# Kernel optimization log

Measured on AMD Instinct MI355X. Metric: run time of the kernel, lower is better.

The kernel has to match this reference:

```python
import jax, jax.numpy as jnp
import numpy as np

N_NODES = 100000
N_REL = 8
F_IN, F_HID, F_OUT = 64, 64, 32
N_EDGES = 1000000


def rgcn_conv(x, W, root, bias, src, dst, edge_type):
    """PyG RGCNConv with default aggr='mean': out[i] = sum_r mean_{j in N_r(i)} W_r x_j + root x_i + bias."""
    R, _, O = W.shape
    N = x.shape[0]
    # Transform every node under every relation: [R, N, O]
    h = jnp.einsum('nf,rfo->rno', x, W)
    # Gather per-edge messages: [E, O]
    msg = h[edge_type, src]
    # Per-(relation, dst) mean aggregation via combined segment ids
    seg = edge_type * N + dst
    sums = jax.ops.segment_sum(msg, seg, num_segments=R * N).reshape(R, N, O)
    cnt = jax.ops.segment_sum(jnp.ones((msg.shape[0],), msg.dtype), seg,
                              num_segments=R * N).reshape(R, N, 1)
    mean = sums / jnp.maximum(cnt, 1.0)  # empty neighborhoods -> 0
    return mean.sum(axis=0) + x @ root + bias


def setup_inputs() -> dict:
    key = jax.random.key(0)
    ks = jax.random.split(key, 9)
    s = lambda fan: 1.0 / np.sqrt(fan)
    x = jax.random.normal(ks[0], (N_NODES, F_IN), jnp.float32)
    edge_index = jax.random.randint(ks[1], (2, N_EDGES), 0, N_NODES, jnp.int64)
    edge_type = jax.random.randint(ks[2], (N_EDGES,), 0, N_REL, jnp.int64)
    W1 = jax.random.normal(ks[3], (N_REL, F_IN, F_HID), jnp.float32) * s(F_IN)
    root1 = jax.random.normal(ks[4], (F_IN, F_HID), jnp.float32) * s(F_IN)
    b1 = jnp.zeros((F_HID,), jnp.float32)
    W2 = jax.random.normal(ks[5], (N_REL, F_HID, F_OUT), jnp.float32) * s(F_HID)
    root2 = jax.random.normal(ks[6], (F_HID, F_OUT), jnp.float32) * s(F_HID)
    b2 = jnp.zeros((F_OUT,), jnp.float32)
    return {"x": x, "W1": W1, "root1": root1, "b1": b1,
            "W2": W2, "root2": root2, "b2": b2,
            "edge_index": edge_index, "edge_type": edge_type}


def reference(x, W1, root1, b1, W2, root2, b2, edge_index, edge_type):
    src, dst = edge_index[0], edge_index[1]
    # encode (dropout is identity in eval mode)
    h = jax.nn.relu(rgcn_conv(x, W1, root1, b1, src, dst, edge_type))
    z = rgcn_conv(h, W2, root2, b2, src, dst, edge_type)
    # decode: gather-dot-product link scores over the same edge list
    return (z[src] * z[dst]).sum(axis=1)
```

## Files before the change

kernel.cpp:

```cpp
#include <hip/hip_runtime.h>

#define F_IN 64
#define F_HID 64
#define F_OUT 32
#define NREL 8
#define SCAP 6144
#define RCAP 10240
#define MAXBUCK 200
#define PA_PE 16

typedef __attribute__((ext_vector_type(8))) short bfrag;
typedef __attribute__((ext_vector_type(4))) float ffrag;

__device__ inline unsigned short f2bf(float f) {
  unsigned u = __float_as_uint(f);
  unsigned r = (u + 0x7fffu + ((u >> 16) & 1u)) >> 16;
  return (unsigned short)r;
}
__device__ inline unsigned bf16pair(float lo, float hi) {
  return (unsigned)f2bf(lo) | ((unsigned)f2bf(hi) << 16);
}
__device__ inline float bflo(unsigned u) { return __uint_as_float(u << 16); }
__device__ inline float bfhi(unsigned u) { return __uint_as_float(u & 0xffff0000u); }

__device__ inline void acc8(float (&acc)[8], float s, uint4 g) {
  acc[0] += s * bflo(g.x); acc[1] += s * bfhi(g.x);
  acc[2] += s * bflo(g.y); acc[3] += s * bfhi(g.y);
  acc[4] += s * bflo(g.z); acc[5] += s * bfhi(g.z);
  acc[6] += s * bflo(g.w); acc[7] += s * bfhi(g.w);
}
__device__ inline float dot8(uint4 a, uint4 b) {
  return bflo(a.x) * bflo(b.x) + bfhi(a.x) * bfhi(b.x) +
         bflo(a.y) * bflo(b.y) + bfhi(a.y) * bfhi(b.y) +
         bflo(a.z) * bflo(b.z) + bfhi(a.z) * bfhi(b.z) +
         bflo(a.w) * bflo(b.w) + bfhi(a.w) * bfhi(b.w);
}

template <int O>
__device__ inline void wprep_one(int t, const float* __restrict__ W,
                                 const float* __restrict__ root,
                                 unsigned short* __restrict__ Wf) {
  constexpr int CT = O / 16;
  int l = t & 63;
  int s = (t >> 6) & 1;
  int rc = t >> 7;
  int c = rc % CT;
  int r = rc / CT;
  const float* wsrc = (r < NREL) ? W + (size_t)r * 64 * O : root;
  unsigned short* dst = Wf + (size_t)t * 8;
  int col = c * 16 + (l & 15);
  int k0 = s * 32 + ((l >> 4) * 8);
#pragma unroll
  for (int j = 0; j < 8; ++j) dst[j] = f2bf(wsrc[(size_t)(k0 + j) * O + col]);
}

__global__ __launch_bounds__(256) void prep_kernel(
    const float* __restrict__ W1, const float* __restrict__ root1,
    const float* __restrict__ W2, const float* __restrict__ root2,
    unsigned short* __restrict__ wf1, unsigned short* __restrict__ wf2,
    int* __restrict__ gcur, int nbuck) {
  int gid = blockIdx.x * 256 + threadIdx.x;
  const int J1 = (NREL + 1) * (F_HID / 16) * 2 * 64;
  const int J2 = (NREL + 1) * (F_OUT / 16) * 2 * 64;
  if (gid < J1) {
    wprep_one<F_HID>(gid, W1, root1, wf1);
  } else if (gid < J1 + J2) {
    wprep_one<F_OUT>(gid - J1, W2, root2, wf2);
  } else if (gid - J1 - J2 < nbuck) {
    int b = gid - J1 - J2;
    gcur[b] = b * SCAP;
  }
}

__global__ __launch_bounds__(256) void binA_kernel(
    const int* __restrict__ src, const int* __restrict__ dst,
    const int* __restrict__ et, int* __restrict__ gcur,
    unsigned* __restrict__ staging, int E) {
  __shared__ int hist[MAXBUCK * 4];
  __shared__ int wbase[MAXBUCK * 4];
  const int tid = threadIdx.x;
  const int wave = tid >> 6;
  for (int i = tid; i < MAXBUCK * 4; i += 256) hist[i] = 0;
  __syncthreads();
  const int base = blockIdx.x * (256 * PA_PE);
  int dv[PA_PE], rk[PA_PE];
#pragma unroll
  for (int j = 0; j < PA_PE; ++j) {
    int e = base + j * 256 + tid;
    if (e < E) {
      int d = dst[e];
      dv[j] = d;
      rk[j] = atomicAdd(&hist[(d >> 9) * 4 + wave], 1);
    } else {
      dv[j] = -1;
    }
  }
  __syncthreads();
  for (int b = tid; b < MAXBUCK; b += 256) {
    int h0 = hist[b * 4 + 0], h1 = hist[b * 4 + 1];
    int h2 = hist[b * 4 + 2], h3 = hist[b * 4 + 3];
    int tot = h0 + h1 + h2 + h3;
    int gb = tot ? atomicAdd(&gcur[b], tot) : 0;
    wbase[b * 4 + 0] = gb;
    wbase[b * 4 + 1] = gb + h0;
    wbase[b * 4 + 2] = gb + h0 + h1;
    wbase[b * 4 + 3] = gb + h0 + h1 + h2;
  }
  __syncthreads();
#pragma unroll
  for (int j = 0; j < PA_PE; ++j) {
    if (dv[j] >= 0) {
      int e = base + j * 256 + tid;
      unsigned pk = (unsigned)src[e] | ((unsigned)et[e] << 17) |
                    ((unsigned)(dv[j] & 511) << 20);
      staging[wbase[(dv[j] >> 9) * 4 + wave] + rk[j]] = pk;
    }
  }
}

__global__ __launch_bounds__(256) void binB_kernel(
    const unsigned* __restrict__ staging, const int* __restrict__ gcur,
    int2* __restrict__ rec, int* __restrict__ startsA, int* __restrict__ endsA,
    int N) {
  __shared__ int cnt8[512 * 8];
  __shared__ int cur[512];
  __shared__ int tsum[256];
  const int b = blockIdx.x;
  const int tid = threadIdx.x;
  const int n0 = b << 9;
  const int nn = min(512, N - n0);
  const int cnt_b = gcur[b] - b * SCAP;
  const unsigned* st = staging + (size_t)b * SCAP;
  for (int i = tid; i < 512 * 8; i += 256) cnt8[i] = 0;
  __syncthreads();
  for (int i = tid; i < cnt_b; i += 256) {
    unsigned e = st[i];
    atomicAdd(&cnt8[((e >> 20) & 511) * 8 + ((e >> 17) & 7)], 1);
  }
  __syncthreads();
  const int na = 2 * tid, nb = 2 * tid + 1;
  int deg0 = 0, deg1 = 0;
#pragma unroll
  for (int r = 0; r < 8; ++r) {
    deg0 += cnt8[na * 8 + r];
    deg1 += cnt8[nb * 8 + r];
  }
  const int pd0 = (deg0 + 7) & ~7, pd1 = (deg1 + 7) & ~7;
  tsum[tid] = pd0 + pd1;
  __syncthreads();
  for (int off = 1; off < 256; off <<= 1) {
    int v = (tid >= off) ? tsum[tid - off] : 0;
    __syncthreads();
    tsum[tid] += v;
    __syncthreads();
  }
  const int excl = tsum[tid] - (pd0 + pd1);
  const int s0 = b * RCAP + excl;
  const int s1 = s0 + pd0;
  if (na < nn) { startsA[n0 + na] = s0; endsA[n0 + na] = s0 + pd0; cur[na] = s0; }
  if (nb < nn) { startsA[n0 + nb] = s1; endsA[n0 + nb] = s1 + pd1; cur[nb] = s1; }
  __syncthreads();
  for (int i = tid; i < 512 * 8; i += 256) {
    int cc = cnt8[i];
    ((float*)cnt8)[i] = cc > 0 ? 1.0f / (float)cc : 0.0f;
  }
  __syncthreads();
  for (int i = tid; i < cnt_b; i += 256) {
    unsigned e = st[i];
    int s = e & 0x1FFFF;
    int r = (e >> 17) & 7;
    int dl = (e >> 20) & 511;
    int pos = atomicAdd(&cur[dl], 1);
    rec[pos] = make_int2(r * N + s, ((const int*)cnt8)[dl * 8 + r]);
  }
  __syncthreads();
  if (na < nn) for (int p = cur[na]; p < s0 + pd0; ++p) rec[p] = make_int2(0, 0);
  if (nb < nn) for (int p = cur[nb]; p < s1 + pd1; ++p) rec[p] = make_int2(0, 0);
}

template <int O, bool F32IN>
__global__ __launch_bounds__(256) void mfma_transform_kernel(
    const void* __restrict__ Xv, const unsigned short* __restrict__ Wf,
    unsigned short* __restrict__ H, int N) {
  constexpr int CT = O / 16;
  constexpr int PAD = (O == 32) ? 40 : 72;
  __shared__ unsigned short tile[64 * PAD];
  const int w = threadIdx.x >> 6;
  const int l = threadIdx.x & 63;
  const int nb = blockIdx.x * 64;
  int arow = nb + w * 16 + (l & 15);
  if (arow >= N) arow = N - 1;
  bfrag a0, a1;
  if (F32IN) {
    const float* xf = (const float*)Xv + (size_t)arow * 64 + ((l >> 4) * 8);
    float4 v0 = *(const float4*)(xf);
    float4 v1 = *(const float4*)(xf + 4);
    float4 v2 = *(const float4*)(xf + 32);
    float4 v3 = *(const float4*)(xf + 36);
    a0[0] = (short)f2bf(v0.x); a0[1] = (short)f2bf(v0.y);
    a0[2] = (short)f2bf(v0.z); a0[3] = (short)f2bf(v0.w);
    a0[4] = (short)f2bf(v1.x); a0[5] = (short)f2bf(v1.y);
    a0[6] = (short)f2bf(v1.z); a0[7] = (short)f2bf(v1.w);
    a1[0] = (short)f2bf(v2.x); a1[1] = (short)f2bf(v2.y);
    a1[2] = (short)f2bf(v2.z); a1[3] = (short)f2bf(v2.w);
    a1[4] = (short)f2bf(v3.x); a1[5] = (short)f2bf(v3.y);
    a1[6] = (short)f2bf(v3.z); a1[7] = (short)f2bf(v3.w);
  } else {
    const unsigned short* xp = (const unsigned short*)Xv + (size_t)arow * 64 + ((l >> 4) * 8);
    a0 = *(const bfrag*)(xp);
    a1 = *(const bfrag*)(xp + 32);
  }
  const int row = threadIdx.x >> 2, seg = threadIdx.x & 3;
  for (int r = 0; r < NREL + 1; ++r) {
    const unsigned short* wb = Wf + ((size_t)r * CT * 2 * 64 + l) * 8;
    ffrag acc[CT];
#pragma unroll
    for (int c = 0; c < CT; ++c) {
      bfrag b0 = *(const bfrag*)(wb + (size_t)(c * 2 + 0) * 512);
      bfrag b1 = *(const bfrag*)(wb + (size_t)(c * 2 + 1) * 512);
      ffrag z = {0.f, 0.f, 0.f, 0.f};
      acc[c] = __builtin_amdgcn_mfma_f32_16x16x32_bf16(a0, b0, z, 0, 0, 0);
      acc[c] = __builtin_amdgcn_mfma_f32_16x16x32_bf16(a1, b1, acc[c], 0, 0, 0);
    }
#pragma unroll
    for (int c = 0; c < CT; ++c)
#pragma unroll
      for (int i = 0; i < 4; ++i)
        tile[(w * 16 + (l >> 4) * 4 + i) * PAD + c * 16 + (l & 15)] = f2bf(acc[c][i]);
    __syncthreads();
    if (nb + row < N) {
      if (O == 64) {
        const uint4* sp = (const uint4*)(tile + row * PAD + seg * 16);
        uint4* gp = (uint4*)(H + ((size_t)r * N + nb + row) * 64 + seg * 16);
        gp[0] = sp[0];
        gp[1] = sp[1];
      } else {
        *(uint4*)(H + ((size_t)r * N + nb + row) * O + seg * 8) =
            *(const uint4*)(tile + row * PAD + seg * 8);
      }
    }
    __syncthreads();
  }
}

template <int O, bool RELU>
__global__ __launch_bounds__(256) void csr_agg_kernel(
    const unsigned* __restrict__ H, const int* __restrict__ startsA,
    const int* __restrict__ endsA, const int2* __restrict__ rec,
    const float* __restrict__ bias, unsigned* __restrict__ Y, int N) {
  constexpr int C = O / 8;
  constexpr int NPB = 256 / C;
  constexpr int HROW = O / 2;
  int t = threadIdx.x;
  int n = blockIdx.x * NPB + t / C;
  int c = t % C;
  if (n >= N) return;
  float acc[8];
  uint4 rr = *(const uint4*)(H + ((size_t)(NREL * N) + n) * HROW + c * 4);
  acc[0] = bias[c * 8 + 0] + bflo(rr.x);
  acc[1] = bias[c * 8 + 1] + bfhi(rr.x);
  acc[2] = bias[c * 8 + 2] + bflo(rr.y);
  acc[3] = bias[c * 8 + 3] + bfhi(rr.y);
  acc[4] = bias[c * 8 + 4] + bflo(rr.z);
  acc[5] = bias[c * 8 + 5] + bfhi(rr.z);
  acc[6] = bias[c * 8 + 6] + bflo(rr.w);
  acc[7] = bias[c * 8 + 7] + bfhi(rr.w);
  int p = startsA[n];
  int end = endsA[n];
  for (; p < end; p += 8) {
    int4 e01 = *(const int4*)(rec + p);
    int4 e23 = *(const int4*)(rec + p + 2);
    int4 e45 = *(const int4*)(rec + p + 4);
    int4 e67 = *(const int4*)(rec + p + 6);
    uint4 g0 = *(const uint4*)(H + (size_t)e01.x * HROW + c * 4);
    uint4 g1 = *(const uint4*)(H + (size_t)e01.z * HROW + c * 4);
    uint4 g2 = *(const uint4*)(H + (size_t)e23.x * HROW + c * 4);
    uint4 g3 = *(const uint4*)(H + (size_t)e23.z * HROW + c * 4);
    uint4 g4 = *(const uint4*)(H + (size_t)e45.x * HROW + c * 4);
    uint4 g5 = *(const uint4*)(H + (size_t)e45.z * HROW + c * 4);
    uint4 g6 = *(const uint4*)(H + (size_t)e67.x * HROW + c * 4);
    uint4 g7 = *(const uint4*)(H + (size_t)e67.z * HROW + c * 4);
    acc8(acc, __int_as_float(e01.y), g0);
    acc8(acc, __int_as_float(e01.w), g1);
    acc8(acc, __int_as_float(e23.y), g2);
    acc8(acc, __int_as_float(e23.w), g3);
    acc8(acc, __int_as_float(e45.y), g4);
    acc8(acc, __int_as_float(e45.w), g5);
    acc8(acc, __int_as_float(e67.y), g6);
    acc8(acc, __int_as_float(e67.w), g7);
  }
  if (RELU) {
#pragma unroll
    for (int j = 0; j < 8; ++j) acc[j] = fmaxf(acc[j], 0.f);
  }
  uint4 o;
  o.x = bf16pair(acc[0], acc[1]);
  o.y = bf16pair(acc[2], acc[3]);
  o.z = bf16pair(acc[4], acc[5]);
  o.w = bf16pair(acc[6], acc[7]);
  *(uint4*)(Y + (size_t)n * HROW + c * 4) = o;
}

__global__ __launch_bounds__(256) void decode_kernel(
    const unsigned* __restrict__ Z, const int* __restrict__ src,
    const int* __restrict__ dst, float* __restrict__ out, int E) {
  int e = blockIdx.x * blockDim.x + threadIdx.x;
  if (e >= E) return;
  const uint4* zs = (const uint4*)(Z + (size_t)src[e] * 16);
  const uint4* zd = (const uint4*)(Z + (size_t)dst[e] * 16);
  uint4 a0 = zs[0], a1 = zs[1], a2 = zs[2], a3 = zs[3];
  uint4 b0 = zd[0], b1 = zd[1], b2 = zd[2], b3 = zd[3];
  out[e] = dot8(a0, b0) + dot8(a1, b1) + dot8(a2, b2) + dot8(a3, b3);
}

extern "C" void kernel_launch(void* const* d_in, const int* in_sizes, int n_in,
                              void* d_out, int out_size, void* d_ws, size_t ws_size,
                              hipStream_t stream) {
  const float* x     = (const float*)d_in[0];
  const float* W1    = (const float*)d_in[1];
  const float* root1 = (const float*)d_in[2];
  const float* b1    = (const float*)d_in[3];
  const float* W2    = (const float*)d_in[4];
  const float* root2 = (const float*)d_in[5];
  const float* b2    = (const float*)d_in[6];
  const int*   ei    = (const int*)d_in[7];
  const int*   et    = (const int*)d_in[8];

  const int N = in_sizes[0] / F_IN;
  const int E = in_sizes[8];
  const int nbuck = (N + 511) >> 9;
  const int* srcp = ei;
  const int* dstp = ei + E;

  char* ws = (char*)d_ws;
  int*            gcur    = (int*)(ws + 0);
  unsigned*       staging = (unsigned*)(ws + 4096);
  int*            startsA = (int*)(ws + 4919296);
  int*            endsA   = (int*)(ws + 5319296);
  int2*           rec     = (int2*)(ws + 5719296);
  unsigned short* wf1     = (unsigned short*)(ws + 21775616);
  unsigned short* wf2     = (unsigned short*)(ws + 21849344);
  unsigned short* h       = (unsigned short*)(ws + 21886208);
  unsigned short* hmid    = (unsigned short*)(ws + 137086208);
  unsigned short* z       = (unsigned short*)(ws + 149886208);

  prep_kernel<<<28, 256, 0, stream>>>(W1, root1, W2, root2, wf1, wf2, gcur, nbuck);
  binA_kernel<<<(E + 256 * PA_PE - 1) / (256 * PA_PE), 256, 0, stream>>>(
      srcp, dstp, et, gcur, staging, E);
  binB_kernel<<<nbuck, 256, 0, stream>>>(staging, gcur, rec, startsA, endsA, N);

  mfma_transform_kernel<F_HID, true>
      <<<(N + 63) / 64, 256, 0, stream>>>(x, wf1, h, N);
  csr_agg_kernel<F_HID, true>
      <<<(N + 31) / 32, 256, 0, stream>>>((const unsigned*)h, startsA, endsA, rec,
                                          b1, (unsigned*)hmid, N);

  mfma_transform_kernel<F_OUT, false>
      <<<(N + 63) / 64, 256, 0, stream>>>(hmid, wf2, h, N);
  csr_agg_kernel<F_OUT, false>
      <<<(N + 63) / 64, 256, 0, stream>>>((const unsigned*)h, startsA, endsA, rec,
                                          b2, (unsigned*)z, N);

  decode_kernel<<<(E + 255) / 256, 256, 0, stream>>>((const unsigned*)z, srcp, dstp,
                                                     (float*)d_out, E);
}
```

Baseline: 174.2 us.

## Store MFMA outputs directly in permuted column layout, dropping LDS staging

The transform kernel now writes MFMA accumulators straight to global memory in an interleaved feature order, which removes the shared-memory tile and both block barriers per relation. Downstream consumers are adapted: layer-2 weights get their K dimension permuted to match layer-1's permuted hidden layout, and the aggregation kernel reads the bias through the same permutation. The trade is narrower global stores (8 or 4 bytes per lane) in exchange for no LDS round trip or synchronization. It relies on the decode dot product being invariant to the permuted output column order.

Measured after the change: 169.5 us. 2.7% less time.

```diff
diff --git a/kernel.cpp b/kernel.cpp
--- a/kernel.cpp
+++ b/kernel.cpp
@@ -36,7 +36,7 @@
          bflo(a.w) * bflo(b.w) + bfhi(a.w) * bfhi(b.w);
 }
 
-template <int O>
+template <int O, bool PERMK>
 __device__ inline void wprep_one(int t, const float* __restrict__ W,
                                  const float* __restrict__ root,
                                  unsigned short* __restrict__ Wf) {
@@ -51,7 +51,11 @@
   int col = c * 16 + (l & 15);
   int k0 = s * 32 + ((l >> 4) * 8);
 #pragma unroll
-  for (int j = 0; j < 8; ++j) dst[j] = f2bf(wsrc[(size_t)(k0 + j) * O + col]);
+  for (int j = 0; j < 8; ++j) {
+    int k = k0 + j;
+    if (PERMK) k = (k & 3) * 16 + (k >> 2);
+    dst[j] = f2bf(wsrc[(size_t)k * O + col]);
+  }
 }
 
 __global__ __launch_bounds__(256) void prep_kernel(
@@ -63,9 +67,9 @@
   const int J1 = (NREL + 1) * (F_HID / 16) * 2 * 64;
   const int J2 = (NREL + 1) * (F_OUT / 16) * 2 * 64;
   if (gid < J1) {
-    wprep_one<F_HID>(gid, W1, root1, wf1);
+    wprep_one<F_HID, false>(gid, W1, root1, wf1);
   } else if (gid < J1 + J2) {
-    wprep_one<F_OUT>(gid - J1, W2, root2, wf2);
+    wprep_one<F_OUT, true>(gid - J1, W2, root2, wf2);
   } else if (gid - J1 - J2 < nbuck) {
     int b = gid - J1 - J2;
     gcur[b] = b * SCAP;
@@ -183,8 +187,6 @@
     const void* __restrict__ Xv, const unsigned short* __restrict__ Wf,
     unsigned short* __restrict__ H, int N) {
   constexpr int CT = O / 16;
-  constexpr int PAD = (O == 32) ? 40 : 72;
-  __shared__ unsigned short tile[64 * PAD];
   const int w = threadIdx.x >> 6;
   const int l = threadIdx.x & 63;
   const int nb = blockIdx.x * 64;
@@ -210,7 +212,7 @@
     a0 = *(const bfrag*)(xp);
     a1 = *(const bfrag*)(xp + 32);
   }
-  const int row = threadIdx.x >> 2, seg = threadIdx.x & 3;
+  const int rbase = nb + w * 16 + ((l >> 4) << 2);
   for (int r = 0; r < NREL + 1; ++r) {
     const unsigned short* wb = Wf + ((size_t)r * CT * 2 * 64 + l) * 8;
     ffrag acc[CT];
@@ -223,23 +225,20 @@
       acc[c] = __builtin_amdgcn_mfma_f32_16x16x32_bf16(a1, b1, acc[c], 0, 0, 0);
     }
 #pragma unroll
-    for (int c = 0; c < CT; ++c)
-#pragma unroll
-      for (int i = 0; i < 4; ++i)
-        tile[(w * 16 + (l >> 4) * 4 + i) * PAD + c * 16 + (l & 15)] = f2bf(acc[c][i]);
-    __syncthreads();
-    if (nb + row < N) {
-      if (O == 64) {
-        const uint4* sp = (const uint4*)(tile + row * PAD + seg * 16);
-        uint4* gp = (uint4*)(H + ((size_t)r * N + nb + row) * 64 + seg * 16);
-        gp[0] = sp[0];
-        gp[1] = sp[1];
-      } else {
-        *(uint4*)(H + ((size_t)r * N + nb + row) * O + seg * 8) =
-            *(const uint4*)(tile + row * PAD + seg * 8);
+    for (int i = 0; i < 4; ++i) {
+      int row = rbase + i;
+      if (row < N) {
+        if (O == 64) {
+          uint2 v;
+          v.x = bf16pair(acc[0][i], acc[1][i]);
+          v.y = bf16pair(acc[2][i], acc[3][i]);
+          *(uint2*)(H + ((size_t)r * N + row) * 64 + (l & 15) * 4) = v;
+        } else {
+          *(unsigned*)(H + ((size_t)r * N + row) * 32 + (l & 15) * 2) =
+              bf16pair(acc[0][i], acc[1][i]);
+        }
       }
     }
-    __syncthreads();
   }
 }
 
@@ -251,20 +250,22 @@
   constexpr int C = O / 8;
   constexpr int NPB = 256 / C;
   constexpr int HROW = O / 2;
+  constexpr int CT = O / 16;
   int t = threadIdx.x;
   int n = blockIdx.x * NPB + t / C;
   int c = t % C;
   if (n >= N) return;
   float acc[8];
   uint4 rr = *(const uint4*)(H + ((size_t)(NREL * N) + n) * HROW + c * 4);
-  acc[0] = bias[c * 8 + 0] + bflo(rr.x);
-  acc[1] = bias[c * 8 + 1] + bfhi(rr.x);
-  acc[2] = bias[c * 8 + 2] + bflo(rr.y);
-  acc[3] = bias[c * 8 + 3] + bfhi(rr.y);
-  acc[4] = bias[c * 8 + 4] + bflo(rr.z);
-  acc[5] = bias[c * 8 + 5] + bfhi(rr.z);
-  acc[6] = bias[c * 8 + 6] + bflo(rr.w);
-  acc[7] = bias[c * 8 + 7] + bfhi(rr.w);
+#pragma unroll
+  for (int j = 0; j < 8; ++j) {
+    int q = c * 8 + j;
+    acc[j] = bias[(q % CT) * 16 + q / CT];
+  }
+  acc[0] += bflo(rr.x); acc[1] += bfhi(rr.x);
+  acc[2] += bflo(rr.y); acc[3] += bfhi(rr.y);
+  acc[4] += bflo(rr.z); acc[5] += bfhi(rr.z);
+  acc[6] += bflo(rr.w); acc[7] += bfhi(rr.w);
   int p = startsA[n];
   int end = endsA[n];
   for (; p < end; p += 8) {
```
